# Optimization experiments

Hardware: AMD Instinct MI355X
Metric: run time of the kernel (lower is better)

The kernel has to match this reference:

```python
import jax, jax.numpy as jnp
import numpy as np

PHI = 1.618033988749895
TWO_PI = float(2.0 * np.pi)
LUT_SIZE = 4096


def _lut_tables():
    ang = jnp.arange(LUT_SIZE, dtype=jnp.float32) * jnp.float32(TWO_PI / LUT_SIZE)
    return jnp.sin(ang), jnp.cos(ang)


def _lookup_sin_cos(theta, sin_t, cos_t):
    # periodic LUT lookup with linear interpolation (differentiable wrt theta)
    pos = theta * jnp.float32(LUT_SIZE / TWO_PI)
    i0 = jnp.floor(pos)
    frac = pos - i0
    idx0 = jnp.mod(i0.astype(jnp.int32), LUT_SIZE)
    idx1 = jnp.mod(idx0 + 1, LUT_SIZE)
    s = sin_t[idx0] * (1.0 - frac) + sin_t[idx1] * frac
    c = cos_t[idx0] * (1.0 - frac) + cos_t[idx1] * frac
    return s, c


def _wrap(t):
    return jnp.mod(t, jnp.float32(TWO_PI))


def _complex_linear(xr, xi, wr, wi):
    return xr @ wr - xi @ wi, xr @ wi + xi @ wr


def _resonant_layer(xr, xi, t, win_r, win_i, wout_r, wout_i, w, b, sin_t, cos_t):
    ur, ui = _complex_linear(xr, xi, win_r, win_i)          # (B, N)
    wavelength = 1.0 + jnp.abs(w)                            # (N,)
    theta = _wrap(t)[:, None] / wavelength + b               # (B, N), wrap_time=True
    s, c = _lookup_sin_cos(theta, sin_t, cos_t)
    vr = ur * c - ui * s                                     # rotate by e^{i*theta}
    vi = ur * s + ui * c
    vr = vr * jax.nn.sigmoid(vr)                             # swish on real/imag parts
    vi = vi * jax.nn.sigmoid(vi)
    return _complex_linear(vr, vi, wout_r, wout_i)


def _forward(input_ids, emb, win_r, win_i, wout_r, wout_i, lw, lb, out_wr, out_wi):
    B, S = input_ids.shape
    D = emb.shape[1] // 2
    sin_t, cos_t = _lut_tables()
    e = emb[input_ids]                         # (B, S, 2D)
    w_emb = jnp.moveaxis(e[..., :D], 1, 0)     # (S, B, D)
    b_emb = jnp.moveaxis(e[..., D:], 1, 0)     # (S, B, D)
    t_idx = jnp.arange(S, dtype=jnp.float32)

    def step(carry, inp):
        hr, hi = carry
        w_t, b_t, t = inp
        wavelength = 1.0 + jnp.abs(w_t)
        t_phi = _wrap(t * jnp.float32(PHI))
        th_r = hr / wavelength + b_t + t_phi
        th_i = hi / wavelength + b_t + t_phi
        sr, cr = _lookup_sin_cos(th_r, sin_t, cos_t)
        si, ci = _lookup_sin_cos(th_i, sin_t, cos_t)
        return (cr * ci - sr * si, cr * si + sr * ci), None

    h0 = jnp.zeros((B, D), jnp.float32)
    (hr, hi), _ = jax.lax.scan(step, (h0, h0), (w_emb, b_emb, t_idx))

    # In the original loop, x is recomputed from h each step and only the last
    # timestep's x reaches output_proj, so layers need only run once at t = S-1.
    t_last = jnp.full((B,), jnp.float32((S - 1) * PHI))
    xr, xi = hr, hi
    for l in range(lw.shape[0]):
        xr, xi = _resonant_layer(xr, xi, t_last, win_r[l], win_i[l],
                                 wout_r[l], wout_i[l], lw[l], lb[l], sin_t, cos_t)
    lr, li = _complex_linear(xr, xi, out_wr, out_wi)
    return lr + li


def setup_inputs() -> dict:
    key = jax.random.key(0)
    ks = jax.random.split(key, 10)
    V, NSIG, D, L, N = 32000, 32000, 64, 2, 128
    B, S = 64, 4096
    input_ids = jax.random.randint(ks[0], (B, S), 0, V)
    emb = jax.random.normal(ks[1], (V, 2 * D), jnp.float32) * (0.02 * 0.5)
    sc_in = float(1.0 / np.sqrt(D))
    sc_out = float(1.0 / np.sqrt(N))
    win_r = jax.random.normal(ks[2], (L, D, N), jnp.float32) * sc_in
    win_i = jax.random.normal(ks[3], (L, D, N), jnp.float32) * sc_in
    wout_r = jax.random.normal(ks[4], (L, N, D), jnp.float32) * sc_out
    wout_i = jax.random.normal(ks[5], (L, N, D), jnp.float32) * sc_out
    lw = jax.random.normal(ks[6], (L, N), jnp.float32)
    lb = jax.random.normal(ks[7], (L, N), jnp.float32)
    out_wr = jax.random.normal(ks[8], (D, NSIG), jnp.float32) * sc_in
    out_wi = jax.random.normal(ks[9], (D, NSIG), jnp.float32) * sc_in
    return {"input_ids": input_ids, "emb": emb, "win_r": win_r, "win_i": win_i,
            "wout_r": wout_r, "wout_i": wout_i, "lw": lw, "lb": lb,
            "out_wr": out_wr, "out_wi": out_wi}


def reference(input_ids, emb, win_r, win_i, wout_r, wout_i, lw, lb, out_wr, out_wi):
    return _forward(input_ids, emb, win_r, win_i, wout_r, wout_i, lw, lb, out_wr, out_wi)
```

## Files before the change

### kernel.cpp

```cpp
#include <hip/hip_runtime.h>
#include <math.h>

#define S_LEN 4096
#define B_SZ  64
#define D_SZ  64
#define N_SZ  128
#define L_SZ  2
#define NSIG  32000

#define TILE   128
#define NT     (S_LEN / TILE)
#define KSTEPS 512
#define KT     (KSTEPS / TILE)
#define T0     (NT - KT)
#define T0S    (T0 * TILE)
#define GRP    16
#define PWAVES 4
#define PSTEPS (TILE / PWAVES)

#define PHI_F     1.6180339887498949f
#define TWO_PI_F  6.2831853071795862f
#define INV_PI_F  0.31830988618379067f
#define SQ2_I2PI  0.22507907903927651f

__global__ __launch_bounds__(PWAVES * 64 + 64, 1) void scan_fused(
    const int*   __restrict__ ids,
    const float* __restrict__ emb,
    float2*      __restrict__ xf)
{
    __shared__ float  s_t2[KSTEPS];
    __shared__ float2 sAC[2][TILE][D_SZ];

    const int b    = blockIdx.x;
    const int tidx = threadIdx.x;
    const int wv   = tidx >> 6;
    const int lane = tidx & 63;

    const int* __restrict__ ids_b = ids + b * S_LEN;

    for (int i = tidx; i < KSTEPS; i += (PWAVES + 1) * 64)
        s_t2[i] = fmodf((float)(T0S + i) * PHI_F, TWO_PI_F) * INV_PI_F + 0.125f;
    __syncthreads();

#define FILL(BUF, TLE) do {                                                  \
    const int t0_ = (TLE) * TILE + (wv - 1) * PSTEPS;          \
    const int s0_ = (wv - 1) * PSTEPS;                                       \
    _Pragma("unroll")                                                        \
    for (int jj = 0; jj < PSTEPS; ++jj) {                                    \
        int   row_ = ids_b[t0_ + jj] << 7;                                   \
        float t2_  = s_t2[t0_ + jj - T0S];                                   \
        float w_   = emb[row_ + lane];                                       \
        float bb_  = emb[row_ + 64 + lane];                                  \
        float A_   = SQ2_I2PI * __builtin_amdgcn_rcpf(1.0f + fabsf(w_));     \
        float bm_  = bb_ * INV_PI_F;                                         \
        asm("" : "+v"(bm_));                 \
        float C_   = bm_ + t2_;                                              \
        sAC[BUF][s0_ + jj][lane] = make_float2(A_, C_);                      \
    }                                                                        \
} while (0)

#define LOADG(R, BUF, G) do {                                                \
    _Pragma("unroll")                                                        \
    for (int j = 0; j < GRP; ++j) R[j] = sAC[BUF][(G) * GRP + j][lane];      \
} while (0)

#define COMPG(R) do {                                                        \
    _Pragma("unroll")                                                        \
    for (int j = 0; j < GRP; ++j) {                                          \
        q = fmaf(u, R[j].x, R[j].y);                                         \
        u = __builtin_amdgcn_sinf(q);                                        \
    }                                                                        \
} while (0)

#define CONSUME(BUF) do {                                                    \
    float2 rA[GRP], rB[GRP];                                                 \
    LOADG(rA, BUF, 0);                                                       \
    LOADG(rB, BUF, 1); COMPG(rA);                                            \
    LOADG(rA, BUF, 2); COMPG(rB);                                            \
    LOADG(rB, BUF, 3); COMPG(rA);                                            \
    LOADG(rA, BUF, 4); COMPG(rB);                                            \
    LOADG(rB, BUF, 5); COMPG(rA);                                            \
    LOADG(rA, BUF, 6); COMPG(rB);                                            \
    LOADG(rB, BUF, 7); COMPG(rA);                                            \
    COMPG(rB);                                                               \
} while (0)

    float u = 0.0f, q = 0.0f;

    if (wv > 0) FILL(0, T0);
    __syncthreads();

    for (int t = T0; t < NT; ++t) {
        const int cur = (t - T0) & 1;
        if (wv > 0) {
            if (t + 1 < NT) FILL(cur ^ 1, t + 1);
        } else {
            CONSUME(cur);
        }
        __syncthreads();
    }

    if (wv == 0) {
        float pr = q - 0.125f;
        xf[b * 64 + lane] = make_float2(__builtin_amdgcn_cosf(pr),
                                        __builtin_amdgcn_sinf(pr));
    }

#undef FILL
#undef LOADG
#undef COMPG
#undef CONSUME
}

__global__ __launch_bounds__(128) void layers_kernel(
    const float2* __restrict__ xf,
    const float*  __restrict__ win_r,
    const float*  __restrict__ win_i,
    const float*  __restrict__ wout_r,
    const float*  __restrict__ wout_i,
    const float*  __restrict__ lw,
    const float*  __restrict__ lb,
    float2*       __restrict__ xpm)
{
    const int b = blockIdx.x;
    const int n = threadIdx.x;

    __shared__ float s_xr[D_SZ], s_xi[D_SZ];
    __shared__ float s_vr[N_SZ], s_vi[N_SZ];

    if (n < D_SZ) {
        float2 v = xf[b * D_SZ + n];
        s_xr[n] = v.x;
        s_xi[n] = v.y;
    }
    __syncthreads();

    const float t_last = (float)(4095.0 * 1.618033988749895);
    const float t_wrap = fmodf(t_last, TWO_PI_F);

    for (int l = 0; l < L_SZ; ++l) {
        float ur = 0.0f, ui = 0.0f;
        const float* wr = win_r + l * D_SZ * N_SZ;
        const float* wi = win_i + l * D_SZ * N_SZ;
        for (int dd = 0; dd < D_SZ; ++dd) {
            float xr = s_xr[dd], xi = s_xi[dd];
            float ar = wr[dd * N_SZ + n], ai = wi[dd * N_SZ + n];
            ur = fmaf(xr, ar, fmaf(-xi, ai, ur));
            ui = fmaf(xr, ai, fmaf( xi, ar, ui));
        }
        float lam = 1.0f + fabsf(lw[l * N_SZ + n]);
        float th  = t_wrap / lam + lb[l * N_SZ + n];
        float sn  = sinf(th), cs = cosf(th);
        float vr  = ur * cs - ui * sn;
        float vi  = ur * sn + ui * cs;
        vr = vr / (1.0f + expf(-vr));
        vi = vi / (1.0f + expf(-vi));
        s_vr[n] = vr;
        s_vi[n] = vi;
        __syncthreads();

        float yr = 0.0f, yi = 0.0f;
        if (n < D_SZ) {
            const float* orp = wout_r + l * N_SZ * D_SZ;
            const float* oip = wout_i + l * N_SZ * D_SZ;
            for (int j = 0; j < N_SZ; ++j) {
                float vr2 = s_vr[j], vi2 = s_vi[j];
                float br = orp[j * D_SZ + n], bi = oip[j * D_SZ + n];
                yr = fmaf(vr2, br, fmaf(-vi2, bi, yr));
                yi = fmaf(vr2, bi, fmaf( vi2, br, yi));
            }
        }
        __syncthreads();
        if (n < D_SZ) {
            s_xr[n] = yr;
            s_xi[n] = yi;
        }
        __syncthreads();
    }

    if (n < D_SZ) {
        xpm[n * B_SZ + b] = make_float2(s_xr[n] + s_xi[n],
                                        s_xr[n] - s_xi[n]);
    }
}

__global__ __launch_bounds__(256, 4) void proj_kernel(
    const float2* __restrict__ xpm,
    const float*  __restrict__ owr,
    const float*  __restrict__ owi,
    float*        __restrict__ out)
{
    const int chunk = blockIdx.x & 127;
    const int oct   = blockIdx.x >> 7;
    if (chunk >= 125) return;

    const int t    = threadIdx.x;
    const int wvq  = t >> 6;
    const int lane = t & 63;
    const int v0   = chunk * 256 + lane * 4;
    const int b0   = oct << 3;

    __shared__ float2 s_x[D_SZ][8];
    __shared__ float  red[4][64][33];

    const float* pwr = owr + (size_t)(wvq * 16) * NSIG + v0;
    const float* pwi = owi + (size_t)(wvq * 16) * NSIG + v0;

    float4 wr0, wi0, wr1, wi1, wr2, wi2, wr3, wi3;

#define LDW(WR, WI, DD) do {                                                 \
    WR = *reinterpret_cast<const float4*>(pwr + (DD) * NSIG);                \
    WI = *reinterpret_cast<const float4*>(pwi + (DD) * NSIG);                \
} while (0)

    LDW(wr0, wi0, 0);
    LDW(wr1, wi1, 1);
    LDW(wr2, wi2, 2);
    LDW(wr3, wi3, 3);

    for (int i = t; i < D_SZ * 8; i += 256)
        s_x[i >> 3][i & 7] = xpm[(i >> 3) * B_SZ + b0 + (i & 7)];
    __syncthreads();

    float acc[8][4];
    #pragma unroll
    for (int bi = 0; bi < 8; ++bi)
        #pragma unroll
        for (int vi = 0; vi < 4; ++vi) acc[bi][vi] = 0.0f;

#define CMP(WR, WI, DD) do {                                                 \
    const int dg_ = wvq * 16 + (DD);                                         \
    _Pragma("unroll")                                                        \
    for (int pb = 0; pb < 4; ++pb) {                                         \
        float4 x_ = *reinterpret_cast<const float4*>(&s_x[dg_][pb * 2]);     \
        const float p0 = x_.x, m0 = x_.y, p1 = x_.z, m1 = x_.w;              \
        acc[2*pb  ][0] = fmaf(WR.x, p0, fmaf(WI.x, m0, acc[2*pb  ][0]));     \
        acc[2*pb  ][1] = fmaf(WR.y, p0, fmaf(WI.y, m0, acc[2*pb  ][1]));     \
        acc[2*pb  ][2] = fmaf(WR.z, p0, fmaf(WI.z, m0, acc[2*pb  ][2]));     \
        acc[2*pb  ][3] = fmaf(WR.w, p0, fmaf(WI.w, m0, acc[2*pb  ][3]));     \
        acc[2*pb+1][0] = fmaf(WR.x, p1, fmaf(WI.x, m1, acc[2*pb+1][0]));     \
        acc[2*pb+1][1] = fmaf(WR.y, p1, fmaf(WI.y, m1, acc[2*pb+1][1]));     \
        acc[2*pb+1][2] = fmaf(WR.z, p1, fmaf(WI.z, m1, acc[2*pb+1][2]));     \
        acc[2*pb+1][3] = fmaf(WR.w, p1, fmaf(WI.w, m1, acc[2*pb+1][3]));     \
    }                                                                        \
} while (0)

    CMP(wr0, wi0, 0);  LDW(wr0, wi0, 4);
    CMP(wr1, wi1, 1);  LDW(wr1, wi1, 5);
    CMP(wr2, wi2, 2);  LDW(wr2, wi2, 6);
    CMP(wr3, wi3, 3);  LDW(wr3, wi3, 7);
    CMP(wr0, wi0, 4);  LDW(wr0, wi0, 8);
    CMP(wr1, wi1, 5);  LDW(wr1, wi1, 9);
    CMP(wr2, wi2, 6);  LDW(wr2, wi2, 10);
    CMP(wr3, wi3, 7);  LDW(wr3, wi3, 11);
    CMP(wr0, wi0, 8);  LDW(wr0, wi0, 12);
    CMP(wr1, wi1, 9);  LDW(wr1, wi1, 13);
    CMP(wr2, wi2, 10); LDW(wr2, wi2, 14);
    CMP(wr3, wi3, 11); LDW(wr3, wi3, 15);
    CMP(wr0, wi0, 12);
    CMP(wr1, wi1, 13);
    CMP(wr2, wi2, 14);
    CMP(wr3, wi3, 15);

#undef LDW
#undef CMP

    #pragma unroll
    for (int bi = 0; bi < 8; ++bi)
        #pragma unroll
        for (int vi = 0; vi < 4; ++vi)
            red[wvq][lane][bi * 4 + vi] = acc[bi][vi];
    __syncthreads();

    float o[8];
    #pragma unroll
    for (int j = 0; j < 8; ++j) {
        const int k = wvq * 8 + j;
        o[j] = ((red[0][lane][k] + red[1][lane][k]) +
                (red[2][lane][k] + red[3][lane][k]));
    }
    *reinterpret_cast<float4*>(out + (size_t)(b0 + 2 * wvq)     * NSIG + v0) =
        make_float4(o[0], o[1], o[2], o[3]);
    *reinterpret_cast<float4*>(out + (size_t)(b0 + 2 * wvq + 1) * NSIG + v0) =
        make_float4(o[4], o[5], o[6], o[7]);
}

extern "C" void kernel_launch(void* const* d_in, const int* in_sizes, int n_in,
                              void* d_out, int out_size, void* d_ws, size_t ws_size,
                              hipStream_t stream)
{
    const int*   ids    = (const int*)  d_in[0];
    const float* emb    = (const float*)d_in[1];
    const float* win_r  = (const float*)d_in[2];
    const float* win_i  = (const float*)d_in[3];
    const float* wout_r = (const float*)d_in[4];
    const float* wout_i = (const float*)d_in[5];
    const float* lw     = (const float*)d_in[6];
    const float* lb     = (const float*)d_in[7];
    const float* owr    = (const float*)d_in[8];
    const float* owi    = (const float*)d_in[9];
    float*       out    = (float*)d_out;

    float2* xf  = (float2*)d_ws;
    float2* xpm = (float2*)((char*)d_ws + 32 * 1024);

    const int nthreads = (PWAVES + 1) * 64;
    scan_fused<<<B_SZ, nthreads, 0, stream>>>(ids, emb, xf);
    layers_kernel<<<B_SZ, 128, 0, stream>>>(xf, win_r, win_i, wout_r, wout_i,
                                            lw, lb, xpm);
    proj_kernel<<<1024, 256, 0, stream>>>(xpm, owr, owi, out);
}
```

Before: 44.64 us.

## Prefetch output weights into cache and shrink proj reduction LDS buffer

Result: slower. 48.41 us (+8.5%).

```diff
diff --git a/kernel.cpp b/kernel.cpp
--- a/kernel.cpp
+++ b/kernel.cpp
@@ -22,6 +22,21 @@
 #define TWO_PI_F  6.2831853071795862f
 #define INV_PI_F  0.31830988618379067f
 #define SQ2_I2PI  0.22507907903927651f
+
+__global__ __launch_bounds__(256) void warm_kernel(
+    const float4* __restrict__ a,
+    const float4* __restrict__ b,
+    int n4)
+{
+    int i = blockIdx.x * 256 + threadIdx.x;
+    const int stride = gridDim.x * 256;
+    for (; i < n4; i += stride) {
+        float4 x = a[i];
+        float4 y = b[i];
+        float s = (x.x + x.y) + (x.z + x.w) + (y.x + y.y) + (y.z + y.w);
+        asm volatile("" :: "v"(s));
+    }
+}
 
 __global__ __launch_bounds__(PWAVES * 64 + 64, 1) void scan_fused(
     const int*   __restrict__ ids,
@@ -201,7 +216,7 @@
     const int b0   = oct << 3;
 
     __shared__ float2 s_x[D_SZ][8];
-    __shared__ float  red[4][64][33];
+    __shared__ float  red[4][64][9];
 
     const float* pwr = owr + (size_t)(wvq * 16) * NSIG + v0;
     const float* pwi = owi + (size_t)(wvq * 16) * NSIG + v0;
@@ -266,23 +281,24 @@
 #undef CMP
 
     #pragma unroll
-    for (int bi = 0; bi < 8; ++bi)
+    for (int r = 0; r < 4; ++r) {
         #pragma unroll
-        for (int vi = 0; vi < 4; ++vi)
-            red[wvq][lane][bi * 4 + vi] = acc[bi][vi];
-    __syncthreads();
-
-    float o[8];
-    #pragma unroll
-    for (int j = 0; j < 8; ++j) {
-        const int k = wvq * 8 + j;
-        o[j] = ((red[0][lane][k] + red[1][lane][k]) +
-                (red[2][lane][k] + red[3][lane][k]));
-    }
-    *reinterpret_cast<float4*>(out + (size_t)(b0 + 2 * wvq)     * NSIG + v0) =
-        make_float4(o[0], o[1], o[2], o[3]);
-    *reinterpret_cast<float4*>(out + (size_t)(b0 + 2 * wvq + 1) * NSIG + v0) =
-        make_float4(o[4], o[5], o[6], o[7]);
+        for (int j = 0; j < 8; ++j)
+            red[wvq][lane][j] = acc[2 * r + (j >> 2)][j & 3];
+        __syncthreads();
+        if (wvq == r) {
+            float o[8];
+            #pragma unroll
+            for (int j = 0; j < 8; ++j)
+                o[j] = ((red[0][lane][j] + red[1][lane][j]) +
+                        (red[2][lane][j] + red[3][lane][j]));
+            *reinterpret_cast<float4*>(out + (size_t)(b0 + 2 * r)     * NSIG + v0) =
+                make_float4(o[0], o[1], o[2], o[3]);
+            *reinterpret_cast<float4*>(out + (size_t)(b0 + 2 * r + 1) * NSIG + v0) =
+                make_float4(o[4], o[5], o[6], o[7]);
+        }
+        __syncthreads();
+    }
 }
 
 extern "C" void kernel_launch(void* const* d_in, const int* in_sizes, int n_in,
@@ -305,6 +321,8 @@
     float2* xpm = (float2*)((char*)d_ws + 32 * 1024);
 
     const int nthreads = (PWAVES + 1) * 64;
+    warm_kernel<<<2048, 256, 0, stream>>>((const float4*)owr, (const float4*)owi,
+                                          (int)((size_t)D_SZ * NSIG / 4));
     scan_fused<<<B_SZ, nthreads, 0, stream>>>(ids, emb, xf);
     layers_kernel<<<B_SZ, 128, 0, stream>>>(xf, win_r, win_i, wout_r, wout_i,
                                             lw, lb, xpm);
```
